# Optimization experiments

Measured on AMD Instinct MI355X. Metric: run time of the kernel, lower is better.

## Reference

```python
import jax, jax.numpy as jnp
import numpy as np

B, N, H, D, L = 4, 1024, 8, 256, 4
SVD, NSP = 16, 512
DK = D // H
EPS = 1e-6


def setup_inputs() -> dict:
    key = jax.random.key(0)
    ks = jax.random.split(key, 40)
    p = {}
    p["x"] = jax.random.normal(ks[0], (B, N, D), jnp.float32)
    p["in_degrees"] = jax.random.randint(ks[1], (N,), 0, N)
    p["out_degrees"] = jax.random.randint(ks[2], (N,), 0, N)
    p["spatial_pos"] = jax.random.randint(ks[3], (N, N), 0, NSP)
    p["svd_emb"] = jax.random.normal(ks[4], (N, 2 * SVD), jnp.float32)
    # embedding tables (padding_idx=0 -> zero row)
    p["in_deg_emb"] = (0.02 * jax.random.normal(ks[5], (N, D), jnp.float32)).at[0].set(0.0)
    p["out_deg_emb"] = (0.02 * jax.random.normal(ks[6], (N, D), jnp.float32)).at[0].set(0.0)
    p["spatial_emb"] = (0.02 * jax.random.normal(ks[7], (NSP, H), jnp.float32)).at[0].set(0.0)
    # SVD linear (stored [in, out]; y = x @ W + b)
    p["W_svd"] = 0.02 * jax.random.normal(ks[8], (2 * SVD, D), jnp.float32)
    p["b_svd"] = jnp.zeros((D,), jnp.float32)
    # per-layer stacked transformer params
    names = ["Wq", "Wk", "Wv", "Wa", "W1", "W2"]
    for i, nm in enumerate(names):
        p[nm] = 0.05 * jax.random.normal(ks[9 + i], (L, D, D), jnp.float32)
    for nm in ["bq", "bk", "bv", "ba", "b1", "b2", "ln1_b", "ln2_b"]:
        p[nm] = jnp.zeros((L, D), jnp.float32)
    p["ln1_g"] = jnp.ones((L, D), jnp.float32)
    p["ln2_g"] = jnp.ones((L, D), jnp.float32)
    return p


def _ln(x, g, b):
    mu = jnp.mean(x, axis=-1, keepdims=True)
    var = jnp.mean(jnp.square(x - mu), axis=-1, keepdims=True)
    return (x - mu) * jax.lax.rsqrt(var + EPS) * g + b


def _forward(x, svd_emb, W_svd, b_svd, in_deg_emb, out_deg_emb, spatial_emb,
             Wq, bq, Wk, bk, Wv, bv, Wa, ba, ln1_g, ln1_b,
             W1, b1, W2, b2, ln2_g, ln2_b,
             in_degrees, out_degrees, spatial_pos):
    # node-level: degree embeddings ([N,D] broadcasts over batch)
    x = x + in_deg_emb[in_degrees] + out_deg_emb[out_degrees]
    # node-level: SVD embedding (deterministic sign = +1 -> concat(u, -v))
    pos = jnp.concatenate([svd_emb[:, :SVD], -svd_emb[:, SVD:]], axis=-1)
    x = x + pos @ W_svd + b_svd
    # attention-level spatial bias: [N,N,H] -> [H,N,N], broadcast over batch
    attn_bias = jnp.transpose(spatial_emb[spatial_pos], (2, 0, 1))
    scale = 1.0 / jnp.sqrt(jnp.asarray(DK, x.dtype))

    def body(h, params):
        wq, bq_, wk, bk_, wv, bv_, wa, ba_, g1, b1_, w1, bb1, w2, bb2, g2, b2_ = params
        q = (h @ wq + bq_).reshape(B, N, H, DK)
        k = (h @ wk + bk_).reshape(B, N, H, DK)
        v = (h @ wv + bv_).reshape(B, N, H, DK)
        # scores [B,H,N,N] + spatial bias [H,N,N]
        scores = jnp.einsum('bqhd,bkhd->bhqk', q, k) * scale + attn_bias
        attn = jax.nn.softmax(scores, axis=-1)
        o = jnp.einsum('bhqk,bkhd->bqhd', attn, v).reshape(B, N, D)
        h = _ln(h + o @ wa + ba_, g1, b1_)
        f = jnp.maximum(h @ w1 + bb1, 0.0) @ w2 + bb2
        h = _ln(h + f, g2, b2_)
        return h, None

    x, _ = jax.lax.scan(body, x, (Wq, bq, Wk, bk, Wv, bv, Wa, ba, ln1_g, ln1_b,
                                  W1, b1, W2, b2, ln2_g, ln2_b))
    return x


def reference(x, svd_emb, W_svd, b_svd, in_deg_emb, out_deg_emb, spatial_emb,
              Wq, bq, Wk, bk, Wv, bv, Wa, ba, ln1_g, ln1_b,
              W1, b1, W2, b2, ln2_g, ln2_b,
              in_degrees, out_degrees, spatial_pos):
    return _forward(x, svd_emb, W_svd, b_svd, in_deg_emb, out_deg_emb, spatial_emb,
                    Wq, bq, Wk, bk, Wv, bv, Wa, ba, ln1_g, ln1_b,
                    W1, b1, W2, b2, ln2_g, ln2_b,
                    in_degrees, out_degrees, spatial_pos)
```

## Files before the change

### kernel.cpp

```cpp
#include <hip/hip_runtime.h>
#include <hip/hip_bf16.h>
#include <math.h>

#define NN 1024
#define BB 4
#define HH 8
#define DD 256
#define LL 4
#define DKK 32
#define MM 4096
#define EPSF 1e-6f

typedef __attribute__((ext_vector_type(8))) short short8;
typedef __attribute__((ext_vector_type(4))) float f32x4;

__device__ __forceinline__ unsigned short f2bf(float f) {
    __hip_bfloat16 h = __float2bfloat16(f);
    return *(unsigned short*)&h;
}
__device__ __forceinline__ float bf2f(unsigned short u) {
    unsigned v = ((unsigned)u) << 16;
    return __builtin_bit_cast(float, v);
}

__global__ __launch_bounds__(256) void init_kernel(
    const float* __restrict__ x, const int* __restrict__ deg_in,
    const int* __restrict__ deg_out, const float* __restrict__ svd,
    const float* __restrict__ in_emb, const float* __restrict__ out_emb,
    const float* __restrict__ Wsvd, const float* __restrict__ bsvd,
    const float* __restrict__ Wq, const float* __restrict__ Wk,
    const float* __restrict__ Wv, const float* __restrict__ Wa,
    const float* __restrict__ W1, const float* __restrict__ W2,
    const int* __restrict__ sp, const float* __restrict__ spemb,
    float* __restrict__ h, short* __restrict__ hb,
    short* __restrict__ Wt, short* __restrict__ bsw)
{
    int blk = blockIdx.x;
    int tid = threadIdx.x;
    {
        int n = blk & (NN - 1);
        int di = deg_in[n], dou = deg_out[n];
        float acc = x[(size_t)blk * DD + tid] + in_emb[(size_t)di * DD + tid]
                  + out_emb[(size_t)dou * DD + tid] + bsvd[tid];
        const float* sv = &svd[n * 32];
#pragma unroll
        for (int j = 0; j < 32; ++j) {
            float v = sv[j];
            v = (j < 16) ? v : -v;
            acc += v * Wsvd[j * DD + tid];
        }
        h[(size_t)blk * DD + tid] = acc;
        hb[(size_t)blk * DD + tid] = (short)f2bf(acc);
    }
    if (blk < 384) {
        __shared__ float t[64][65];
        int z = blk >> 4, tile = blk & 15;
        int name = z >> 2;
        const float* srcs[6] = {Wq, Wk, Wv, Wa, W1, W2};
        const float* W = srcs[name] + (size_t)(z & 3) * DD * DD;
        short* dst = Wt + (size_t)z * DD * DD;
        int r0 = (tile >> 2) * 64, c0 = (tile & 3) * 64;
#pragma unroll
        for (int i = 0; i < 16; ++i) {
            int idx = i * 256 + tid;
            int r = idx >> 6, cc = idx & 63;
            t[r][cc] = W[(size_t)(r0 + r) * DD + c0 + cc];
        }
        __syncthreads();
#pragma unroll
        for (int i = 0; i < 16; ++i) {
            int idx = i * 256 + tid;
            int n = idx >> 6, k = idx & 63;
            dst[(size_t)(c0 + n) * DD + r0 + k] = (short)f2bf(t[k][n]);
        }
    } else if (blk < 640) {
        int tt = (blk - 384) * 256 + tid;
        int ln = tt & 63, kt = (tt >> 6) & 15, q16 = tt >> 10;
        int qd = ln >> 4, cc = ln & 15;
        unsigned buf[8][8];
#pragma unroll
        for (int j = 0; j < 16; ++j) {
            int f = j >> 2, r = j & 3;
            int row = q16 * 16 + qd * 4 + r;
            int col = kt * 64 + f * 16 + cc;
            int pp = sp[row * NN + col];
#pragma unroll
            for (int hh = 0; hh < 8; ++hh) {
                unsigned short u = f2bf(spemb[pp * 8 + hh]);
                if (j & 1) buf[hh][j >> 1] |= ((unsigned)u) << 16;
                else       buf[hh][j >> 1] = u;
            }
        }
#pragma unroll
        for (int hh = 0; hh < 8; ++hh) {
            uint4* dst = (uint4*)&bsw[(((size_t)hh * 64 + q16) * 16 + kt) * 1024 + (size_t)ln * 16];
            dst[0] = make_uint4(buf[hh][0], buf[hh][1], buf[hh][2], buf[hh][3]);
            dst[1] = make_uint4(buf[hh][4], buf[hh][5], buf[hh][6], buf[hh][7]);
        }
    }
}

__global__ __launch_bounds__(256) void gemm_qkv_kernel(
    const short* __restrict__ A,
    const short* __restrict__ Wtq, const short* __restrict__ Wtk,
    const short* __restrict__ Wtv,
    const float* __restrict__ bq, const float* __restrict__ bk,
    const float* __restrict__ bv,
    short* __restrict__ qo, short* __restrict__ ko, short* __restrict__ vo)
{
    int z = blockIdx.z;
    const short* Wt = (z == 0) ? Wtq : (z == 1) ? Wtk : Wtv;
    const float* bs = (z == 0) ? bq : (z == 1) ? bk : bv;
    int tid = threadIdx.x, wave = tid >> 6, lane = tid & 63;
    int quad = lane >> 4, c = lane & 15;
    int m0 = blockIdx.x * 16;
    int n0 = blockIdx.y * 64 + wave * 16;
    f32x4 acc = {0.f, 0.f, 0.f, 0.f};
    const short* Ap = &A[(size_t)(m0 + c) * DD];
#pragma unroll
    for (int ks = 0; ks < 8; ++ks) {
        short8 af = *(const short8*)&Ap[ks * 32 + quad * 8];
        short8 bf = *(const short8*)&Wt[(size_t)(n0 + c) * DD + ks * 32 + quad * 8];
        acc = __builtin_amdgcn_mfma_f32_16x16x32_bf16(af, bf, acc, 0, 0, 0);
    }
    int b = m0 >> 10;
    int tok0 = (m0 & (NN - 1)) + quad * 4;
    int col = n0 + c;
    int head = col >> 5, dk = col & 31;
    int bh = b * 8 + head;
    float bv2 = bs[col];
    const float scale = 0.17677669529663687f;
    if (z == 2) {
        ushort4 pk;
        pk.x = f2bf(acc[0] + bv2); pk.y = f2bf(acc[1] + bv2);
        pk.z = f2bf(acc[2] + bv2); pk.w = f2bf(acc[3] + bv2);
        *(ushort4*)&vo[((size_t)bh * DKK + dk) * NN + tok0] = pk;
    } else {
        short* out = (z == 0) ? qo : ko;
        float sc = (z == 0) ? scale : 1.0f;
#pragma unroll
        for (int r = 0; r < 4; ++r)
            out[((size_t)bh * NN + tok0 + r) * DKK + dk] =
                (short)f2bf((acc[r] + bv2) * sc);
    }
}

template <int QKV>
__global__ __launch_bounds__(512) void layer_kernel(
    const short* __restrict__ q, const short* __restrict__ k,
    const short* __restrict__ vt, const short* __restrict__ bsw,
    const short* __restrict__ Wta, const short* __restrict__ Wt1,
    const short* __restrict__ Wt2,
    const float* __restrict__ ba, const float* __restrict__ b1,
    const float* __restrict__ b2,
    const float* __restrict__ g1, const float* __restrict__ lb1,
    const float* __restrict__ g2, const float* __restrict__ lb2,
    float* __restrict__ h,
    const short* __restrict__ Wtqn, const short* __restrict__ Wtkn,
    const short* __restrict__ Wtvn,
    const float* __restrict__ bqn, const float* __restrict__ bkn,
    const float* __restrict__ bvn,
    short* __restrict__ qo, short* __restrict__ ko, short* __restrict__ vo)
{
    int tid = threadIdx.x, wave = tid >> 6, lane = tid & 63;
    int quad = lane >> 4, c = lane & 15;
    int m0 = blockIdx.x * 16;
    int b = m0 >> 10;
    int q0 = m0 & (NN - 1);
    int qt_idx = q0 >> 4;
    int head = wave;
    int bh = b * 8 + head;
    int nb = wave * 32;

    __shared__ short Pl[8][16][72];
    __shared__ short t_in[16][264];
    __shared__ short t1s[16][264];
    __shared__ float shs[8][16][2];
    const f32x4 zero = {0.f, 0.f, 0.f, 0.f};

    {
        short (*P)[72] = Pl[wave];
        short8 qf = *(const short8*)&q[((size_t)bh * NN + q0 + c) * DKK + quad * 8];
        f32x4 Oa0 = zero, Oa1 = zero;
        float lsum[4] = {0.f, 0.f, 0.f, 0.f};

        short8 kf[4];
#pragma unroll
        for (int f = 0; f < 4; ++f)
            kf[f] = *(const short8*)&k[((size_t)bh * NN + f * 16 + c) * DKK + quad * 8];

        for (int kti = 0; kti < 16; ++kti) {
            int kt = kti * 64;
            f32x4 s[4];
#pragma unroll
            for (int f = 0; f < 4; ++f)
                s[f] = __builtin_amdgcn_mfma_f32_16x16x32_bf16(qf, kf[f], zero, 0, 0, 0);
            if (kti < 15) {
#pragma unroll
                for (int f = 0; f < 4; ++f)
                    kf[f] = *(const short8*)&k[((size_t)bh * NN + kt + 64 + f * 16 + c) * DKK + quad * 8];
            }
            short8 vf0[2], vf1[2];
#pragma unroll
            for (int kc = 0; kc < 2; ++kc) {
                vf0[kc] = *(const short8*)&vt[((size_t)bh * DKK + 0  + c) * NN + kt + kc * 32 + quad * 8];
                vf1[kc] = *(const short8*)&vt[((size_t)bh * DKK + 16 + c) * NN + kt + kc * 32 + quad * 8];
            }
            const short* bp = &bsw[(((size_t)head * 64 + qt_idx) * 16 + kti) * 1024 + (size_t)lane * 16];
            short8 b0 = *(const short8*)bp;
            short8 b1v = *(const short8*)(bp + 8);
#pragma unroll
            for (int f = 0; f < 4; ++f)
#pragma unroll
                for (int r = 0; r < 4; ++r) {
                    int jj = f * 4 + r;
                    unsigned short uu = (unsigned short)((jj < 8) ? b0[jj] : b1v[jj - 8]);
                    float p = __expf(s[f][r] + bf2f(uu));
                    s[f][r] = p;
                    lsum[r] += p;
                }
#pragma unroll
            for (int f = 0; f < 4; ++f)
#pragma unroll
                for (int r = 0; r < 4; ++r)
                    P[quad * 4 + r][f * 16 + c] = (short)f2bf(s[f][r]);
#pragma unroll
            for (int kc = 0; kc < 2; ++kc) {
                short8 pf = *(const short8*)&P[c][kc * 32 + quad * 8];
                Oa0 = __builtin_amdgcn_mfma_f32_16x16x32_bf16(pf, vf0[kc], Oa0, 0, 0, 0);
                Oa1 = __builtin_amdgcn_mfma_f32_16x16x32_bf16(pf, vf1[kc], Oa1, 0, 0, 0);
            }
        }
#pragma unroll
        for (int r = 0; r < 4; ++r)
#pragma unroll
            for (int off = 1; off < 16; off <<= 1)
                lsum[r] += __shfl_xor(lsum[r], off);
#pragma unroll
        for (int r = 0; r < 4; ++r) {
            float invl = 1.0f / lsum[r];
            int rr = quad * 4 + r;
            t_in[rr][head * 32 + c]      = (short)f2bf(Oa0[r] * invl);
            t_in[rr][head * 32 + 16 + c] = (short)f2bf(Oa1[r] * invl);
        }
    }
    __syncthreads();

    f32x4 acc[2] = {zero, zero};
#pragma unroll
    for (int ks = 0; ks < 8; ++ks) {
        short8 af = *(const short8*)&t_in[c][ks * 32 + quad * 8];
#pragma unroll
        for (int f = 0; f < 2; ++f) {
            short8 bf = *(const short8*)&Wta[(size_t)(nb + f * 16 + c) * DD + ks * 32 + quad * 8];
            acc[f] = __builtin_amdgcn_mfma_f32_16x16x32_bf16(af, bf, acc[f], 0, 0, 0);
        }
    }
    float val[2][4];
    float ps[4] = {0.f,0.f,0.f,0.f}, ps2[4] = {0.f,0.f,0.f,0.f};
#pragma unroll
    for (int f = 0; f < 2; ++f) {
        int col = nb + f * 16 + c;
        float bv = ba[col];
#pragma unroll
        for (int r = 0; r < 4; ++r) {
            float v = h[(size_t)(m0 + quad * 4 + r) * DD + col] + acc[f][r] + bv;
            val[f][r] = v;
            ps[r] += v;
            ps2[r] += v * v;
        }
    }
#pragma unroll
    for (int r = 0; r < 4; ++r)
#pragma unroll
        for (int off = 1; off < 16; off <<= 1) {
            ps[r]  += __shfl_xor(ps[r], off);
            ps2[r] += __shfl_xor(ps2[r], off);
        }
    if (c == 0)
#pragma unroll
        for (int r = 0; r < 4; ++r) {
            shs[wave][quad * 4 + r][0] = ps[r];
            shs[wave][quad * 4 + r][1] = ps2[r];
        }
    __syncthreads();
    float res[2][4];
#pragma unroll
    for (int r = 0; r < 4; ++r) {
        int rr = quad * 4 + r;
        float ts = 0.f, t2 = 0.f;
#pragma unroll
        for (int w = 0; w < 8; ++w) { ts += shs[w][rr][0]; t2 += shs[w][rr][1]; }
        float mu = ts * (1.0f / DD);
        float rv = rsqrtf(t2 * (1.0f / DD) - mu * mu + EPSF);
#pragma unroll
        for (int f = 0; f < 2; ++f) {
            int col = nb + f * 16 + c;
            float nv = (val[f][r] - mu) * rv * g1[col] + lb1[col];
            res[f][r] = nv;
            t_in[rr][col] = (short)f2bf(nv);
        }
    }
    __syncthreads();
#pragma unroll
    for (int f = 0; f < 2; ++f) {
        int n0 = nb + f * 16;
        f32x4 a1 = zero;
#pragma unroll
        for (int ks = 0; ks < 8; ++ks) {
            short8 af = *(const short8*)&t_in[c][ks * 32 + quad * 8];
            short8 bf = *(const short8*)&Wt1[(size_t)(n0 + c) * DD + ks * 32 + quad * 8];
            a1 = __builtin_amdgcn_mfma_f32_16x16x32_bf16(af, bf, a1, 0, 0, 0);
        }
        float bv = b1[n0 + c];
#pragma unroll
        for (int r = 0; r < 4; ++r)
            t1s[quad * 4 + r][n0 + c] = (short)f2bf(fmaxf(a1[r] + bv, 0.f));
    }
    __syncthreads();
    f32x4 acc2[2] = {zero, zero};
#pragma unroll
    for (int ks = 0; ks < 8; ++ks) {
        short8 af = *(const short8*)&t1s[c][ks * 32 + quad * 8];
#pragma unroll
        for (int f = 0; f < 2; ++f) {
            short8 bf = *(const short8*)&Wt2[(size_t)(nb + f * 16 + c) * DD + ks * 32 + quad * 8];
            acc2[f] = __builtin_amdgcn_mfma_f32_16x16x32_bf16(af, bf, acc2[f], 0, 0, 0);
        }
    }
    float ps_2[4] = {0.f,0.f,0.f,0.f}, ps2_2[4] = {0.f,0.f,0.f,0.f};
#pragma unroll
    for (int f = 0; f < 2; ++f) {
        int col = nb + f * 16 + c;
        float bv = b2[col];
#pragma unroll
        for (int r = 0; r < 4; ++r) {
            float v = res[f][r] + acc2[f][r] + bv;
            val[f][r] = v;
            ps_2[r] += v;
            ps2_2[r] += v * v;
        }
    }
#pragma unroll
    for (int r = 0; r < 4; ++r)
#pragma unroll
        for (int off = 1; off < 16; off <<= 1) {
            ps_2[r]  += __shfl_xor(ps_2[r], off);
            ps2_2[r] += __shfl_xor(ps2_2[r], off);
        }
    __syncthreads();
    if (c == 0)
#pragma unroll
        for (int r = 0; r < 4; ++r) {
            shs[wave][quad * 4 + r][0] = ps_2[r];
            shs[wave][quad * 4 + r][1] = ps2_2[r];
        }
    __syncthreads();
#pragma unroll
    for (int r = 0; r < 4; ++r) {
        int rr = quad * 4 + r;
        float ts = 0.f, t2 = 0.f;
#pragma unroll
        for (int w = 0; w < 8; ++w) { ts += shs[w][rr][0]; t2 += shs[w][rr][1]; }
        float mu = ts * (1.0f / DD);
        float rv = rsqrtf(t2 * (1.0f / DD) - mu * mu + EPSF);
#pragma unroll
        for (int f = 0; f < 2; ++f) {
            int col = nb + f * 16 + c;
            float nv = (val[f][r] - mu) * rv * g2[col] + lb2[col];
            h[(size_t)(m0 + rr) * DD + col] = nv;
            t_in[rr][col] = (short)f2bf(nv);
        }
    }
    if (QKV == 0) return;
    __syncthreads();
    {
        int tok0 = q0 + quad * 4;
        const short* Wz[3]  = {Wtqn, Wtkn, Wtvn};
        const float* bz[3]  = {bqn, bkn, bvn};
        const float scale = 0.17677669529663687f;
#pragma unroll
        for (int z = 0; z < 3; ++z) {
#pragma unroll
            for (int f = 0; f < 2; ++f) {
                int n0 = nb + f * 16;
                f32x4 aq = zero;
#pragma unroll
                for (int ks = 0; ks < 8; ++ks) {
                    short8 af = *(const short8*)&t_in[c][ks * 32 + quad * 8];
                    short8 bf = *(const short8*)&Wz[z][(size_t)(n0 + c) * DD + ks * 32 + quad * 8];
                    aq = __builtin_amdgcn_mfma_f32_16x16x32_bf16(af, bf, aq, 0, 0, 0);
                }
                int col = n0 + c;
                int hd = col >> 5, dk = col & 31;
                int bh2 = b * 8 + hd;
                float bv2 = bz[z][col];
                if (z == 2) {
                    ushort4 pk;
                    pk.x = f2bf(aq[0] + bv2); pk.y = f2bf(aq[1] + bv2);
                    pk.z = f2bf(aq[2] + bv2); pk.w = f2bf(aq[3] + bv2);
                    *(ushort4*)&vo[((size_t)bh2 * DKK + dk) * NN + tok0] = pk;
                } else {
                    short* out = (z == 0) ? qo : ko;
                    float sc = (z == 0) ? scale : 1.0f;
#pragma unroll
                    for (int r = 0; r < 4; ++r)
                        out[((size_t)bh2 * NN + tok0 + r) * DKK + dk] =
                            (short)f2bf((aq[r] + bv2) * sc);
                }
            }
        }
    }
}

extern "C" void kernel_launch(void* const* d_in, const int* in_sizes, int n_in,
                              void* d_out, int out_size, void* d_ws, size_t ws_size,
                              hipStream_t stream)
{
    const float* x       = (const float*)d_in[0];
    const int*   deg_in  = (const int*)d_in[1];
    const int*   deg_out = (const int*)d_in[2];
    const int*   sp      = (const int*)d_in[3];
    const float* svd     = (const float*)d_in[4];
    const float* in_emb  = (const float*)d_in[5];
    const float* out_emb = (const float*)d_in[6];
    const float* spemb   = (const float*)d_in[7];
    const float* Wsvd    = (const float*)d_in[8];
    const float* bsvd    = (const float*)d_in[9];
    const float* Wq = (const float*)d_in[10];
    const float* Wk = (const float*)d_in[11];
    const float* Wv = (const float*)d_in[12];
    const float* Wa = (const float*)d_in[13];
    const float* W1 = (const float*)d_in[14];
    const float* W2 = (const float*)d_in[15];
    const float* bq = (const float*)d_in[16];
    const float* bk = (const float*)d_in[17];
    const float* bv = (const float*)d_in[18];
    const float* ba = (const float*)d_in[19];
    const float* b1 = (const float*)d_in[20];
    const float* b2 = (const float*)d_in[21];
    const float* ln1b = (const float*)d_in[22];
    const float* ln2b = (const float*)d_in[23];
    const float* ln1g = (const float*)d_in[24];
    const float* ln2g = (const float*)d_in[25];

    float* h = (float*)d_out;
    char*  ws = (char*)d_ws;
    short* bias = (short*)ws;
    short* qb   = (short*)(ws + ((size_t)16 << 20));
    short* kb   = (short*)(ws + ((size_t)18 << 20));
    short* vtb  = (short*)(ws + ((size_t)20 << 20));
    short* hb   = (short*)(ws + ((size_t)26 << 20));
    short* Wt   = (short*)(ws + ((size_t)28 << 20));

    init_kernel<<<MM, 256, 0, stream>>>(x, deg_in, deg_out, svd, in_emb,
        out_emb, Wsvd, bsvd, Wq, Wk, Wv, Wa, W1, W2, sp, spemb, h, hb, Wt, bias);

    const size_t WSZ = (size_t)DD * DD;
    gemm_qkv_kernel<<<dim3(MM / 16, 4, 3), 256, 0, stream>>>(
        hb, Wt + 0 * WSZ, Wt + 4 * WSZ, Wt + 8 * WSZ, bq, bk, bv, qb, kb, vtb);

    for (int l = 0; l < LL; ++l) {
        const size_t bo = (size_t)l * DD;
        const short* Wta = Wt + (3 * 4 + l) * WSZ;
        const short* Wt1 = Wt + (4 * 4 + l) * WSZ;
        const short* Wt2 = Wt + (5 * 4 + l) * WSZ;

        if (l < LL - 1) {
            const size_t bo_n = (size_t)(l + 1) * DD;
            layer_kernel<1><<<MM / 16, 512, 0, stream>>>(
                qb, kb, vtb, bias, Wta, Wt1, Wt2,
                ba + bo, b1 + bo, b2 + bo,
                ln1g + bo, ln1b + bo, ln2g + bo, ln2b + bo, h,
                Wt + (0 * 4 + l + 1) * WSZ, Wt + (1 * 4 + l + 1) * WSZ,
                Wt + (2 * 4 + l + 1) * WSZ,
                bq + bo_n, bk + bo_n, bv + bo_n, qb, kb, vtb);
        } else {
            layer_kernel<0><<<MM / 16, 512, 0, stream>>>(
                qb, kb, vtb, bias, Wta, Wt1, Wt2,
                ba + bo, b1 + bo, b2 + bo,
                ln1g + bo, ln1b + bo, ln2g + bo, ln2b + bo, h,
                nullptr, nullptr, nullptr, nullptr, nullptr, nullptr,
                nullptr, nullptr, nullptr);
        }
    }
}
```

Baseline: 342.7 us.

## Compute transposed attention scores to feed P to PV MFMA from registers

Swaps the operands of the QK^T MFMA so each lane holds a column of scores, which makes the exponentiated probabilities directly usable as the B operand of 16x16x16 bf16 MFMAs against V^T. This removes the per-wave LDS staging buffer for P along with its write/read round-trip, and reduces the row-sum to two cross-quad shuffles. The spatial-bias swizzle in the init kernel and the output write to t_in are re-indexed to match the transposed layout. The tradeoff is twice as many smaller MFMAs and narrower 8-byte V loads.

Result: slower. 398.9 us (+16.4%).

```diff
diff --git a/kernel.cpp b/kernel.cpp
--- a/kernel.cpp
+++ b/kernel.cpp
@@ -12,7 +12,10 @@
 #define EPSF 1e-6f
 
 typedef __attribute__((ext_vector_type(8))) short short8;
+typedef __attribute__((ext_vector_type(4))) short s16x4;
 typedef __attribute__((ext_vector_type(4))) float f32x4;
+
+#define MFMA16(a, b, c) __builtin_amdgcn_mfma_f32_16x16x16bf16_1k(a, b, c, 0, 0, 0)
 
 __device__ __forceinline__ unsigned short f2bf(float f) {
     __hip_bfloat16 h = __float2bfloat16(f);
@@ -81,8 +84,8 @@
 #pragma unroll
         for (int j = 0; j < 16; ++j) {
             int f = j >> 2, r = j & 3;
-            int row = q16 * 16 + qd * 4 + r;
-            int col = kt * 64 + f * 16 + cc;
+            int row = q16 * 16 + cc;
+            int col = kt * 64 + f * 16 + qd * 4 + r;
             int pp = sp[row * NN + col];
 #pragma unroll
             for (int hh = 0; hh < 8; ++hh) {
@@ -172,17 +175,15 @@
     int bh = b * 8 + head;
     int nb = wave * 32;
 
-    __shared__ short Pl[8][16][72];
     __shared__ short t_in[16][264];
     __shared__ short t1s[16][264];
     __shared__ float shs[8][16][2];
     const f32x4 zero = {0.f, 0.f, 0.f, 0.f};
 
     {
-        short (*P)[72] = Pl[wave];
         short8 qf = *(const short8*)&q[((size_t)bh * NN + q0 + c) * DKK + quad * 8];
         f32x4 Oa0 = zero, Oa1 = zero;
-        float lsum[4] = {0.f, 0.f, 0.f, 0.f};
+        float lsum = 0.f;
 
         short8 kf[4];
 #pragma unroll
@@ -194,54 +195,39 @@
             f32x4 s[4];
 #pragma unroll
             for (int f = 0; f < 4; ++f)
-                s[f] = __builtin_amdgcn_mfma_f32_16x16x32_bf16(qf, kf[f], zero, 0, 0, 0);
+                s[f] = __builtin_amdgcn_mfma_f32_16x16x32_bf16(kf[f], qf, zero, 0, 0, 0);
             if (kti < 15) {
 #pragma unroll
                 for (int f = 0; f < 4; ++f)
                     kf[f] = *(const short8*)&k[((size_t)bh * NN + kt + 64 + f * 16 + c) * DKK + quad * 8];
-            }
-            short8 vf0[2], vf1[2];
-#pragma unroll
-            for (int kc = 0; kc < 2; ++kc) {
-                vf0[kc] = *(const short8*)&vt[((size_t)bh * DKK + 0  + c) * NN + kt + kc * 32 + quad * 8];
-                vf1[kc] = *(const short8*)&vt[((size_t)bh * DKK + 16 + c) * NN + kt + kc * 32 + quad * 8];
             }
             const short* bp = &bsw[(((size_t)head * 64 + qt_idx) * 16 + kti) * 1024 + (size_t)lane * 16];
             short8 b0 = *(const short8*)bp;
             short8 b1v = *(const short8*)(bp + 8);
 #pragma unroll
-            for (int f = 0; f < 4; ++f)
+            for (int f = 0; f < 4; ++f) {
+                s16x4 pf;
 #pragma unroll
                 for (int r = 0; r < 4; ++r) {
                     int jj = f * 4 + r;
                     unsigned short uu = (unsigned short)((jj < 8) ? b0[jj] : b1v[jj - 8]);
                     float p = __expf(s[f][r] + bf2f(uu));
-                    s[f][r] = p;
-                    lsum[r] += p;
+                    lsum += p;
+                    pf[r] = (short)f2bf(p);
                 }
-#pragma unroll
-            for (int f = 0; f < 4; ++f)
-#pragma unroll
-                for (int r = 0; r < 4; ++r)
-                    P[quad * 4 + r][f * 16 + c] = (short)f2bf(s[f][r]);
-#pragma unroll
-            for (int kc = 0; kc < 2; ++kc) {
-                short8 pf = *(const short8*)&P[c][kc * 32 + quad * 8];
-                Oa0 = __builtin_amdgcn_mfma_f32_16x16x32_bf16(pf, vf0[kc], Oa0, 0, 0, 0);
-                Oa1 = __builtin_amdgcn_mfma_f32_16x16x32_bf16(pf, vf1[kc], Oa1, 0, 0, 0);
+                s16x4 va0 = *(const s16x4*)&vt[((size_t)bh * DKK + 0  + c) * NN + kt + f * 16 + quad * 4];
+                s16x4 va1 = *(const s16x4*)&vt[((size_t)bh * DKK + 16 + c) * NN + kt + f * 16 + quad * 4];
+                Oa0 = MFMA16(va0, pf, Oa0);
+                Oa1 = MFMA16(va1, pf, Oa1);
             }
         }
-#pragma unroll
-        for (int r = 0; r < 4; ++r)
-#pragma unroll
-            for (int off = 1; off < 16; off <<= 1)
-                lsum[r] += __shfl_xor(lsum[r], off);
+        lsum += __shfl_xor(lsum, 16);
+        lsum += __shfl_xor(lsum, 32);
+        float invl = 1.0f / lsum;
 #pragma unroll
         for (int r = 0; r < 4; ++r) {
-            float invl = 1.0f / lsum[r];
-            int rr = quad * 4 + r;
-            t_in[rr][head * 32 + c]      = (short)f2bf(Oa0[r] * invl);
-            t_in[rr][head * 32 + 16 + c] = (short)f2bf(Oa1[r] * invl);
+            t_in[c][head * 32 + quad * 4 + r]      = (short)f2bf(Oa0[r] * invl);
+            t_in[c][head * 32 + 16 + quad * 4 + r] = (short)f2bf(Oa1[r] * invl);
         }
     }
     __syncthreads();
```
